# Kernel optimization log

Measured on AMD Instinct MI355X. Metric: run time of the kernel, lower is better.

The kernel has to match this reference:

```python
import jax, jax.numpy as jnp
import numpy as np

N, D = 131072, 128   # total nodes, feature size (input_size)
G, L = 512, 448      # num graphs, max padded segment length
EPS = 1e-5


def setup_inputs() -> dict:
    key = jax.random.key(0)
    ks = jax.random.split(key, 8)
    # ragged segment sizes summing exactly to N, each <= L
    rng = np.random.default_rng(0)
    counts = rng.integers(192, 321, size=G)
    diff = N - int(counts.sum())
    idx = rng.integers(0, G, size=abs(diff))
    np.add.at(counts, idx, 1 if diff > 0 else -1)
    assert int(counts.sum()) == N and int(counts.max()) <= L
    batch = jnp.asarray(np.repeat(np.arange(G), counts), dtype=jnp.int32)

    s = 1.0 / np.sqrt(D)
    x = jax.random.normal(ks[0], (N, D), jnp.float32)
    Wk = jax.random.normal(ks[1], (D, D), jnp.float32) * s
    Wq = jax.random.normal(ks[2], (D, D), jnp.float32) * s
    Wv = jax.random.normal(ks[3], (D, D), jnp.float32) * s
    bk = jnp.zeros((D,), jnp.float32)
    bq = jnp.zeros((D,), jnp.float32)
    bv = jnp.zeros((D,), jnp.float32)
    gamma = jnp.ones((D,), jnp.float32)
    beta = jnp.zeros((D,), jnp.float32)
    return {"x": x, "Wk": Wk, "bk": bk, "Wq": Wq, "bq": bq,
            "Wv": Wv, "bv": bv, "gamma": gamma, "beta": beta, "batch": batch}


def reference(x, Wk, bk, Wq, bq, Wv, bv, gamma, beta, batch):
    keys = x @ Wk.T + bk
    query = x @ Wq.T + bq
    values = x @ Wv.T + bv

    counts = jnp.bincount(batch, length=G)                 # [G]
    starts = jnp.cumsum(counts) - counts                   # segment offsets
    pos = jnp.arange(N, dtype=batch.dtype) - starts[batch]  # index within segment

    # scatter ragged nodes into padded [G, L, D] blocks (honors block-diagonal structure)
    kp = jnp.zeros((G, L, D), x.dtype).at[batch, pos].set(keys)
    qp = jnp.zeros((G, L, D), x.dtype).at[batch, pos].set(query)
    vp = jnp.zeros((G, L, D), x.dtype).at[batch, pos].set(values)
    valid = jnp.arange(L)[None, :] < counts[:, None]        # [G, L]

    # NOTE: original computes softmax(K @ Q^T / sqrt(dk)) @ V (keys as rows)
    scale = 1.0 / jnp.sqrt(jnp.asarray(D, x.dtype))
    scores = jnp.einsum('gld,gmd->glm', kp, qp) * scale     # [G, L, L]
    scores = jnp.where(valid[:, None, :], scores, jnp.asarray(-1e9, x.dtype))
    attn = jax.nn.softmax(scores, axis=-1)
    zp = jnp.einsum('glm,gmd->gld', attn, vp)               # [G, L, D]
    z = zp[batch, pos]                                      # back to ragged [N, D]

    h = x + z
    mu = jnp.mean(h, axis=-1, keepdims=True)
    var = jnp.var(h, axis=-1, keepdims=True)
    return (h - mu) / jnp.sqrt(var + EPS) * gamma + beta
```

## Files before the change

### kernel.cpp

```cpp
#include <hip/hip_runtime.h>
#include <hip/hip_bf16.h>

#define N_NODES 131072
#define DIM 128
#define NG 512

typedef __bf16 bf16;
typedef __attribute__((ext_vector_type(8))) __bf16 bf16x8;
typedef __attribute__((ext_vector_type(4))) float f32x4;

#define WS_STARTS 0
#define WS_WF     8192
#define WS_KB     131072
#define WS_QB     (131072 + 33554432)
#define WS_VTB    (131072 + 2*33554432)

__global__ void seg_starts_kernel(const int* __restrict__ batch, int* __restrict__ starts) {
    int g = threadIdx.x;
    int lo = 0, hi = N_NODES;
    while (lo < hi) { int mid = (lo + hi) >> 1; if (batch[mid] < g) lo = mid + 1; else hi = mid; }
    starts[g] = lo;
    if (g == 0) starts[NG] = N_NODES;
}

__global__ void wconv_kernel(const float* __restrict__ Wk, const float* __restrict__ Wq,
                             const float* __restrict__ Wv, bf16* __restrict__ Wf) {
    int f = blockIdx.x * 256 + threadIdx.x;
    int lane = f & 63, ks = (f >> 6) & 3, n0 = (f >> 8) & 7, mat = f >> 11;
    const float* src = (mat == 0) ? Wk : ((mat == 1) ? Wq : Wv);
    int col = n0 * 16 + (lane & 15);
    int koff = ks * 32 + (lane >> 4) * 8;
    const float* p = src + col * DIM + koff;
    bf16* dst = Wf + (size_t)f * 8;
    #pragma unroll
    for (int j = 0; j < 8; j++) dst[j] = (bf16)p[j];
}

__global__ __launch_bounds__(256) void qkv_kernel(
        const float* __restrict__ x, const bf16* __restrict__ Wf,
        const float* __restrict__ bk, const float* __restrict__ bq, const float* __restrict__ bv,
        bf16* __restrict__ Kb, bf16* __restrict__ Qb, bf16* __restrict__ Vtb) {
    __shared__ bf16 tile[128 * 136];
    const int tid = threadIdx.x;
    const int w = tid >> 6, lane = tid & 63, q = lane >> 4, i = lane & 15;
    const int r0 = blockIdx.x * 128;

    {
        #pragma unroll
        for (int it = 0; it < 16; it++) {
            int e = tid * 4 + it * 1024;
            int row = e >> 7, col = e & 127;
            float4 u = *(const float4*)(x + (size_t)(r0 + row) * DIM + col);
            bf16 b[4] = {(bf16)u.x, (bf16)u.y, (bf16)u.z, (bf16)u.w};
            *(ushort4*)&tile[row * 136 + col] = *(ushort4*)b;
        }
    }
    __syncthreads();

    bf16x8 af[2][4];
    #pragma unroll
    for (int rg = 0; rg < 2; rg++)
        #pragma unroll
        for (int ks = 0; ks < 4; ks++)
            af[rg][ks] = *(const bf16x8*)&tile[(w * 32 + rg * 16 + i) * 136 + ks * 32 + q * 8];
    __syncthreads();

    for (int mat = 0; mat < 3; mat++) {
        const float* bias = (mat == 0) ? bk : ((mat == 1) ? bq : bv);
        for (int n0 = 0; n0 < 8; n0++) {
            int col = n0 * 16 + i;
            float bias_v = bias[col];
            f32x4 acc0 = {0,0,0,0}, acc1 = {0,0,0,0};
            #pragma unroll
            for (int ks = 0; ks < 4; ks++) {
                bf16x8 bw = *(const bf16x8*)(Wf + ((size_t)((mat * 8 + n0) * 4 + ks) * 64 + lane) * 8);
                acc0 = __builtin_amdgcn_mfma_f32_16x16x32_bf16(af[0][ks], bw, acc0, 0, 0, 0);
                acc1 = __builtin_amdgcn_mfma_f32_16x16x32_bf16(af[1][ks], bw, acc1, 0, 0, 0);
            }
            #pragma unroll
            for (int rg = 0; rg < 2; rg++) {
                f32x4 a = rg ? acc1 : acc0;
                #pragma unroll
                for (int r = 0; r < 4; r++) {
                    int rowl = w * 32 + rg * 16 + q * 4 + r;
                    bf16 hv = (bf16)(a[r] + bias_v);
                    if (mat < 2) tile[rowl * 136 + col] = hv;
                    else         tile[col * 136 + rowl] = hv;
                }
            }
        }
        __syncthreads();
        {
            int row = tid >> 1, half = tid & 1;
            const uint4* src = (const uint4*)(tile + row * 136 + half * 64);
            uint4* dst;
            if (mat == 0)      dst = (uint4*)(Kb  + (size_t)(r0 + row) * DIM + half * 64);
            else if (mat == 1) dst = (uint4*)(Qb  + (size_t)(r0 + row) * DIM + half * 64);
            else               dst = (uint4*)(Vtb + (size_t)row * N_NODES + r0 + half * 64);
            #pragma unroll
            for (int j = 0; j < 8; j++) dst[j] = src[j];
        }
        __syncthreads();
    }
}

__global__ __launch_bounds__(256) void attn_kernel(
        const float* __restrict__ x,
        const bf16* __restrict__ Kb, const bf16* __restrict__ Qb, const bf16* __restrict__ Vtb,
        const float* __restrict__ gamma, const float* __restrict__ beta,
        const int* __restrict__ starts, float* __restrict__ out) {
    __shared__ bf16 Qs[64 * 136];
    __shared__ bf16 Vts[128 * 72];

    const int g = blockIdx.y;
    const int seg = starts[g];
    const int c = starts[g + 1] - seg;
    const int l0 = blockIdx.x * 64;
    if (l0 >= c) return;

    const int tid = threadIdx.x;
    const int w = tid >> 6, lane = tid & 63, q = lane >> 4, i = lane & 15;

    bf16x8 afK[4];
    {
        int lrow = l0 + w * 16 + i;
        if (lrow > c - 1) lrow = c - 1;
        const bf16* krow = Kb + (size_t)(seg + lrow) * DIM;
        #pragma unroll
        for (int ks = 0; ks < 4; ks++)
            afK[ks] = *(const bf16x8*)(krow + ks * 32 + q * 8);
    }

    float mi[4], li[4];
    f32x4 Oc[8];
    #pragma unroll
    for (int r = 0; r < 4; r++) { mi[r] = -3.0e38f; li[r] = 0.0f; }
    #pragma unroll
    for (int t = 0; t < 8; t++) Oc[t] = (f32x4){0,0,0,0};

    const float kSc = 0.08838834764831845f * 1.4426950408889634f;

    const int cid0 = seg >> 6, cid1 = (seg + c - 1) >> 6;
    for (int cid = cid0; cid <= cid1; cid++) {
        const int a = cid << 6;
        __syncthreads();
        {
            int row = tid >> 4;
            int col8 = (tid & 15) * 8;
            #pragma unroll
            for (int p = 0; p < 4; p++, row += 16) {
                uint4 v = *(const uint4*)(Qb + (size_t)(a + row) * DIM + col8);
                *(uint4*)&Qs[row * 136 + col8] = v;
            }
        }
        {
            int d = tid >> 3;
            int m8 = (tid & 7) * 8;
            #pragma unroll
            for (int p = 0; p < 4; p++, d += 32) {
                uint4 v = *(const uint4*)(Vtb + (size_t)d * N_NODES + a + m8);
                *(uint4*)&Vts[d * 72 + m8] = v;
            }
        }
        __syncthreads();

        f32x4 s[4];
        #pragma unroll
        for (int ti = 0; ti < 4; ti++) {
            f32x4 acc = {0,0,0,0};
            #pragma unroll
            for (int ks = 0; ks < 4; ks++) {
                bf16x8 bq = *(const bf16x8*)&Qs[(ti * 16 + i) * 136 + ks * 32 + q * 8];
                acc = __builtin_amdgcn_mfma_f32_16x16x32_bf16(afK[ks], bq, acc, 0, 0, 0);
            }
            s[ti] = acc;
        }
        float m4[4] = {-3.0e38f, -3.0e38f, -3.0e38f, -3.0e38f};
        #pragma unroll
        for (int ti = 0; ti < 4; ti++) {
            int mg = a + ti * 16 + i;
            bool valid = (mg >= seg) && (mg < seg + c);
            #pragma unroll
            for (int r = 0; r < 4; r++) {
                float sv = valid ? s[ti][r] * kSc : -1.0e30f;
                s[ti][r] = sv;
                m4[r] = fmaxf(m4[r], sv);
            }
        }
        #pragma unroll
        for (int st = 1; st < 16; st <<= 1)
            #pragma unroll
            for (int r = 0; r < 4; r++)
                m4[r] = fmaxf(m4[r], __shfl_xor(m4[r], st));
        float alpha[4], rs[4];
        #pragma unroll
        for (int r = 0; r < 4; r++) {
            float mn = fmaxf(mi[r], m4[r]);
            alpha[r] = exp2f(mi[r] - mn);
            mi[r] = mn;
            rs[r] = 0.0f;
        }
        #pragma unroll
        for (int ti = 0; ti < 4; ti++)
            #pragma unroll
            for (int r = 0; r < 4; r++) {
                float pv = exp2f(s[ti][r] - mi[r]);
                s[ti][r] = pv;
                rs[r] += pv;
            }
        #pragma unroll
        for (int st = 1; st < 16; st <<= 1)
            #pragma unroll
            for (int r = 0; r < 4; r++)
                rs[r] += __shfl_xor(rs[r], st);
        #pragma unroll
        for (int r = 0; r < 4; r++) li[r] = li[r] * alpha[r] + rs[r];
        #pragma unroll
        for (int t = 0; t < 8; t++)
            #pragma unroll
            for (int r = 0; r < 4; r++)
                Oc[t][r] *= alpha[r];

        __syncthreads();
        bf16* Pw = Qs + w * (16 * 72);
        #pragma unroll
        for (int ti = 0; ti < 4; ti++)
            #pragma unroll
            for (int r = 0; r < 4; r++)
                Pw[(q * 4 + r) * 72 + ti * 16 + i] = (bf16)s[ti][r];

        bf16x8 afP[2];
        #pragma unroll
        for (int k2 = 0; k2 < 2; k2++)
            afP[k2] = *(const bf16x8*)&Pw[i * 72 + k2 * 32 + q * 8];
        #pragma unroll
        for (int dt = 0; dt < 8; dt++) {
            #pragma unroll
            for (int k2 = 0; k2 < 2; k2++) {
                bf16x8 bv = *(const bf16x8*)&Vts[(dt * 16 + i) * 72 + k2 * 32 + q * 8];
                Oc[dt] = __builtin_amdgcn_mfma_f32_16x16x32_bf16(afP[k2], bv, Oc[dt], 0, 0, 0);
            }
        }
    }

    float gv[8], bvv[8];
    #pragma unroll
    for (int ti = 0; ti < 8; ti++) { gv[ti] = gamma[ti * 16 + i]; bvv[ti] = beta[ti * 16 + i]; }
    for (int r = 0; r < 4; r++) {
        int lg = l0 + w * 16 + q * 4 + r;
        if (lg >= c) continue;
        size_t node = (size_t)(seg + lg);
        float inv = 1.0f / li[r];
        const float* xr = x + node * DIM;
        float h[8], sum = 0.0f, ss = 0.0f;
        #pragma unroll
        for (int ti = 0; ti < 8; ti++) {
            float hv = xr[ti * 16 + i] + Oc[ti][r] * inv;
            h[ti] = hv;
            sum += hv; ss += hv * hv;
        }
        #pragma unroll
        for (int st = 1; st < 16; st <<= 1) {
            sum += __shfl_xor(sum, st);
            ss  += __shfl_xor(ss, st);
        }
        float mu = sum * (1.0f / 128.0f);
        float var = ss * (1.0f / 128.0f) - mu * mu;
        float rstd = rsqrtf(var + 1e-5f);
        float* op = out + node * DIM;
        #pragma unroll
        for (int ti = 0; ti < 8; ti++)
            op[ti * 16 + i] = (h[ti] - mu) * rstd * gv[ti] + bvv[ti];
    }
}

extern "C" void kernel_launch(void* const* d_in, const int* in_sizes, int n_in,
                              void* d_out, int out_size, void* d_ws, size_t ws_size,
                              hipStream_t stream) {
    (void)in_sizes; (void)n_in; (void)out_size; (void)ws_size;
    const float* x     = (const float*)d_in[0];
    const float* Wk    = (const float*)d_in[1];
    const float* bk    = (const float*)d_in[2];
    const float* Wq    = (const float*)d_in[3];
    const float* bq    = (const float*)d_in[4];
    const float* Wv    = (const float*)d_in[5];
    const float* bv    = (const float*)d_in[6];
    const float* gamma = (const float*)d_in[7];
    const float* beta  = (const float*)d_in[8];
    const int*   batch = (const int*)d_in[9];
    float* out = (float*)d_out;

    char* ws = (char*)d_ws;
    int*  starts = (int*)(ws + WS_STARTS);
    bf16* Wf  = (bf16*)(ws + WS_WF);
    bf16* Kb  = (bf16*)(ws + WS_KB);
    bf16* Qb  = (bf16*)(ws + WS_QB);
    bf16* Vtb = (bf16*)(ws + WS_VTB);

    seg_starts_kernel<<<1, 512, 0, stream>>>(batch, starts);
    wconv_kernel<<<24, 256, 0, stream>>>(Wk, Wq, Wv, Wf);
    qkv_kernel<<<1024, 256, 0, stream>>>(x, Wf, bk, bq, bv, Kb, Qb, Vtb);
    attn_kernel<<<dim3(7, NG), 256, 0, stream>>>(x, Kb, Qb, Vtb, gamma, beta, starts, out);
}
```

Measured before the change: 296.1 us.

## Drop online-softmax max tracking, fold scale into Wk, split QKV grid

Folds the softmax scale and log2(e) into the K weights and bias, so scores come out of the MFMA already in exp2 domain. The running max, alpha rescaling and per-chunk shuffles are removed, and exponentials are taken directly, which assumes scores stay bounded. Masking runs only on the first and last chunks, chunks start at 8-aligned offsets, P gets its own LDS buffer so one barrier is dropped, and the row-sum reduction moves after the loop. The QKV kernel splits its three matrices across grid.y, and attention uses 512-thread blocks covering 128 rows. Skipping max subtraction risks overflow for large scores.

```diff
diff --git a/kernel.cpp b/kernel.cpp
--- a/kernel.cpp
+++ b/kernel.cpp
@@ -8,6 +8,8 @@
 typedef __bf16 bf16;
 typedef __attribute__((ext_vector_type(8))) __bf16 bf16x8;
 typedef __attribute__((ext_vector_type(4))) float f32x4;
+
+#define KSC 0.12753785006196978f
 
 #define WS_STARTS 0
 #define WS_WF     8192
@@ -28,12 +30,13 @@
     int f = blockIdx.x * 256 + threadIdx.x;
     int lane = f & 63, ks = (f >> 6) & 3, n0 = (f >> 8) & 7, mat = f >> 11;
     const float* src = (mat == 0) ? Wk : ((mat == 1) ? Wq : Wv);
+    float sc = (mat == 0) ? KSC : 1.0f;
     int col = n0 * 16 + (lane & 15);
     int koff = ks * 32 + (lane >> 4) * 8;
     const float* p = src + col * DIM + koff;
     bf16* dst = Wf + (size_t)f * 8;
     #pragma unroll
-    for (int j = 0; j < 8; j++) dst[j] = (bf16)p[j];
+    for (int j = 0; j < 8; j++) dst[j] = (bf16)(p[j] * sc);
 }
 
 __global__ __launch_bounds__(256) void qkv_kernel(
@@ -44,6 +47,7 @@
     const int tid = threadIdx.x;
     const int w = tid >> 6, lane = tid & 63, q = lane >> 4, i = lane & 15;
     const int r0 = blockIdx.x * 128;
+    const int mat = blockIdx.y;
 
     {
         #pragma unroll
@@ -65,57 +69,56 @@
             af[rg][ks] = *(const bf16x8*)&tile[(w * 32 + rg * 16 + i) * 136 + ks * 32 + q * 8];
     __syncthreads();
 
-    for (int mat = 0; mat < 3; mat++) {
-        const float* bias = (mat == 0) ? bk : ((mat == 1) ? bq : bv);
-        for (int n0 = 0; n0 < 8; n0++) {
-            int col = n0 * 16 + i;
-            float bias_v = bias[col];
-            f32x4 acc0 = {0,0,0,0}, acc1 = {0,0,0,0};
-            #pragma unroll
-            for (int ks = 0; ks < 4; ks++) {
-                bf16x8 bw = *(const bf16x8*)(Wf + ((size_t)((mat * 8 + n0) * 4 + ks) * 64 + lane) * 8);
-                acc0 = __builtin_amdgcn_mfma_f32_16x16x32_bf16(af[0][ks], bw, acc0, 0, 0, 0);
-                acc1 = __builtin_amdgcn_mfma_f32_16x16x32_bf16(af[1][ks], bw, acc1, 0, 0, 0);
-            }
-            #pragma unroll
-            for (int rg = 0; rg < 2; rg++) {
-                f32x4 a = rg ? acc1 : acc0;
-                #pragma unroll
-                for (int r = 0; r < 4; r++) {
-                    int rowl = w * 32 + rg * 16 + q * 4 + r;
-                    bf16 hv = (bf16)(a[r] + bias_v);
-                    if (mat < 2) tile[rowl * 136 + col] = hv;
-                    else         tile[col * 136 + rowl] = hv;
-                }
-            }
-        }
-        __syncthreads();
-        {
-            int row = tid >> 1, half = tid & 1;
-            const uint4* src = (const uint4*)(tile + row * 136 + half * 64);
-            uint4* dst;
-            if (mat == 0)      dst = (uint4*)(Kb  + (size_t)(r0 + row) * DIM + half * 64);
-            else if (mat == 1) dst = (uint4*)(Qb  + (size_t)(r0 + row) * DIM + half * 64);
-            else               dst = (uint4*)(Vtb + (size_t)row * N_NODES + r0 + half * 64);
-            #pragma unroll
-            for (int j = 0; j < 8; j++) dst[j] = src[j];
-        }
-        __syncthreads();
-    }
-}
-
-__global__ __launch_bounds__(256) void attn_kernel(
+    const float* bias = (mat == 0) ? bk : ((mat == 1) ? bq : bv);
+    const float bscale = (mat == 0) ? KSC : 1.0f;
+    for (int n0 = 0; n0 < 8; n0++) {
+        int col = n0 * 16 + i;
+        float bias_v = bias[col] * bscale;
+        f32x4 acc0 = {0,0,0,0}, acc1 = {0,0,0,0};
+        #pragma unroll
+        for (int ks = 0; ks < 4; ks++) {
+            bf16x8 bw = *(const bf16x8*)(Wf + ((size_t)((mat * 8 + n0) * 4 + ks) * 64 + lane) * 8);
+            acc0 = __builtin_amdgcn_mfma_f32_16x16x32_bf16(af[0][ks], bw, acc0, 0, 0, 0);
+            acc1 = __builtin_amdgcn_mfma_f32_16x16x32_bf16(af[1][ks], bw, acc1, 0, 0, 0);
+        }
+        #pragma unroll
+        for (int rg = 0; rg < 2; rg++) {
+            f32x4 a = rg ? acc1 : acc0;
+            #pragma unroll
+            for (int r = 0; r < 4; r++) {
+                int rowl = w * 32 + rg * 16 + q * 4 + r;
+                bf16 hv = (bf16)(a[r] + bias_v);
+                if (mat < 2) tile[rowl * 136 + col] = hv;
+                else         tile[col * 136 + rowl] = hv;
+            }
+        }
+    }
+    __syncthreads();
+    {
+        int row = tid >> 1, half = tid & 1;
+        const uint4* src = (const uint4*)(tile + row * 136 + half * 64);
+        uint4* dst;
+        if (mat == 0)      dst = (uint4*)(Kb  + (size_t)(r0 + row) * DIM + half * 64);
+        else if (mat == 1) dst = (uint4*)(Qb  + (size_t)(r0 + row) * DIM + half * 64);
+        else               dst = (uint4*)(Vtb + (size_t)row * N_NODES + r0 + half * 64);
+        #pragma unroll
+        for (int j = 0; j < 8; j++) dst[j] = src[j];
+    }
+}
+
+__global__ __launch_bounds__(512, 6) void attn_kernel(
         const float* __restrict__ x,
         const bf16* __restrict__ Kb, const bf16* __restrict__ Qb, const bf16* __restrict__ Vtb,
         const float* __restrict__ gamma, const float* __restrict__ beta,
         const int* __restrict__ starts, float* __restrict__ out) {
     __shared__ bf16 Qs[64 * 136];
     __shared__ bf16 Vts[128 * 72];
+    __shared__ bf16 Ps[8 * 16 * 72];
 
     const int g = blockIdx.y;
     const int seg = starts[g];
     const int c = starts[g + 1] - seg;
-    const int l0 = blockIdx.x * 64;
+    const int l0 = blockIdx.x * 128;
     if (l0 >= c) return;
 
     const int tid = threadIdx.x;
@@ -131,35 +134,34 @@
             afK[ks] = *(const bf16x8*)(krow + ks * 32 + q * 8);
     }
 
-    float mi[4], li[4];
+    float li[4] = {0.0f, 0.0f, 0.0f, 0.0f};
     f32x4 Oc[8];
     #pragma unroll
-    for (int r = 0; r < 4; r++) { mi[r] = -3.0e38f; li[r] = 0.0f; }
-    #pragma unroll
     for (int t = 0; t < 8; t++) Oc[t] = (f32x4){0,0,0,0};
 
-    const float kSc = 0.08838834764831845f * 1.4426950408889634f;
-
-    const int cid0 = seg >> 6, cid1 = (seg + c - 1) >> 6;
-    for (int cid = cid0; cid <= cid1; cid++) {
-        const int a = cid << 6;
+    const int mstart = seg & ~7;
+    const int nch = (seg - mstart + c + 63) >> 6;
+    for (int mc = 0; mc < nch; mc++) {
+        const int mbase = mstart + (mc << 6);
         __syncthreads();
         {
-            int row = tid >> 4;
-            int col8 = (tid & 15) * 8;
-            #pragma unroll
-            for (int p = 0; p < 4; p++, row += 16) {
-                uint4 v = *(const uint4*)(Qb + (size_t)(a + row) * DIM + col8);
-                *(uint4*)&Qs[row * 136 + col8] = v;
+            int row = tid >> 3;
+            int gr = mbase + row; if (gr > N_NODES - 1) gr = N_NODES - 1;
+            const uint4* src = (const uint4*)(Qb + (size_t)gr * DIM);
+            #pragma unroll
+            for (int p = 0; p < 2; p++) {
+                int slot = (tid & 7) + 8 * p;
+                *(uint4*)&Qs[row * 136 + slot * 8] = src[slot];
             }
         }
         {
-            int d = tid >> 3;
-            int m8 = (tid & 7) * 8;
-            #pragma unroll
-            for (int p = 0; p < 4; p++, d += 32) {
-                uint4 v = *(const uint4*)(Vtb + (size_t)d * N_NODES + a + m8);
-                *(uint4*)&Vts[d * 72 + m8] = v;
+            int d = tid >> 2;
+            #pragma unroll
+            for (int p = 0; p < 2; p++) {
+                int slot = (tid & 3) + 4 * p;
+                int mo = mbase + slot * 8; if (mo > N_NODES - 8) mo = N_NODES - 8;
+                uint4 v = *(const uint4*)(Vtb + (size_t)d * N_NODES + mo);
+                *(uint4*)&Vts[d * 72 + slot * 8] = v;
             }
         }
         __syncthreads();
@@ -175,59 +177,26 @@
             }
             s[ti] = acc;
         }
-        float m4[4] = {-3.0e38f, -3.0e38f, -3.0e38f, -3.0e38f};
-        #pragma unroll
-        for (int ti = 0; ti < 4; ti++) {
-            int mg = a + ti * 16 + i;
-            bool valid = (mg >= seg) && (mg < seg + c);
+        if (mc == 0 || mc == nch - 1) {
+            #pragma unroll
+            for (int ti = 0; ti < 4; ti++) {
+                int mg = mbase + ti * 16 + i;
+                bool valid = (mg >= seg) && (mg < seg + c);
+                #pragma unroll
+                for (int r = 0; r < 4; r++)
+                    s[ti][r] = valid ? s[ti][r] : -1.0e30f;
+            }
+        }
+
+        bf16* Pw = Ps + w * (16 * 72);
+        #pragma unroll
+        for (int ti = 0; ti < 4; ti++)
             #pragma unroll
             for (int r = 0; r < 4; r++) {
-                float sv = valid ? s[ti][r] * kSc : -1.0e30f;
-                s[ti][r] = sv;
-                m4[r] = fmaxf(m4[r], sv);
-            }
-        }
-        #pragma unroll
-        for (int st = 1; st < 16; st <<= 1)
-            #pragma unroll
-            for (int r = 0; r < 4; r++)
-                m4[r] = fmaxf(m4[r], __shfl_xor(m4[r], st));
-        float alpha[4], rs[4];
-        #pragma unroll
-        for (int r = 0; r < 4; r++) {
-            float mn = fmaxf(mi[r], m4[r]);
-            alpha[r] = exp2f(mi[r] - mn);
-            mi[r] = mn;
-            rs[r] = 0.0f;
-        }
-        #pragma unroll
-        for (int ti = 0; ti < 4; ti++)
-            #pragma unroll
-            for (int r = 0; r < 4; r++) {
-                float pv = exp2f(s[ti][r] - mi[r]);
-                s[ti][r] = pv;
-                rs[r] += pv;
-            }
-        #pragma unroll
-        for (int st = 1; st < 16; st <<= 1)
-            #pragma unroll
-            for (int r = 0; r < 4; r++)
-                rs[r] += __shfl_xor(rs[r], st);
-        #pragma unroll
-        for (int r = 0; r < 4; r++) li[r] = li[r] * alpha[r] + rs[r];
-        #pragma unroll
-        for (int t = 0; t < 8; t++)
-            #pragma unroll
-            for (int r = 0; r < 4; r++)
-                Oc[t][r] *= alpha[r];
-
-        __syncthreads();
-        bf16* Pw = Qs + w * (16 * 72);
-        #pragma unroll
-        for (int ti = 0; ti < 4; ti++)
-            #pragma unroll
-            for (int r = 0; r < 4; r++)
-                Pw[(q * 4 + r) * 72 + ti * 16 + i] = (bf16)s[ti][r];
+                float pv = exp2f(s[ti][r]);
+                li[r] += pv;
+                Pw[(q * 4 + r) * 72 + ti * 16 + i] = (bf16)pv;
+            }
 
         bf16x8 afP[2];
         #pragma unroll
@@ -242,6 +211,12 @@
             }
         }
     }
+
+    #pragma unroll
+    for (int st = 1; st < 16; st <<= 1)
+        #pragma unroll
+        for (int r = 0; r < 4; r++)
+            li[r] += __shfl_xor(li[r], st);
 
     float gv[8], bvv[8];
     #pragma unroll
@@ -299,6 +274,6 @@
 
     seg_starts_kernel<<<1, 512, 0, stream>>>(batch, starts);
     wconv_kernel<<<24, 256, 0, stream>>>(Wk, Wq, Wv, Wf);
-    qkv_kernel<<<1024, 256, 0, stream>>>(x, Wf, bk, bq, bv, Kb, Qb, Vtb);
-    attn_kernel<<<dim3(7, NG), 256, 0, stream>>>(x, Kb, Qb, Vtb, gamma, beta, starts, out);
-}
+    qkv_kernel<<<dim3(1024, 3), 256, 0, stream>>>(x, Wf, bk, bq, bv, Kb, Qb, Vtb);
+    attn_kernel<<<dim3(4, NG), 512, 0, stream>>>(x, Kb, Qb, Vtb, gamma, beta, starts, out);
+}
```

After: 416.4 us. +40.6%, slower.
